# Performance work log

Measured on AMD Instinct MI355X. Metric: run time of the kernel, lower is better.

The kernel has to match this reference:

```python
import jax, jax.numpy as jnp
import numpy as np

B, S, H = 8, 2048, 512
M = 4096
TEMP = 0.1
EPS = 1e-6


def setup_inputs() -> dict:
    key = jax.random.key(0)
    ks = jax.random.split(key, 8)
    scale = 1.0 / np.sqrt(H)
    return {
        "hidden_states": jax.random.normal(ks[0], (B, S, H), dtype=jnp.float32),
        "memory_keys": jax.random.normal(ks[1], (M, H), dtype=jnp.float32),
        "memory_values": jax.random.normal(ks[2], (M, H), dtype=jnp.float32),
        "Wk": jax.random.normal(ks[3], (H, H), dtype=jnp.float32) * scale,
        "bk": jnp.zeros((H,), dtype=jnp.float32),
        "Wo": jax.random.normal(ks[4], (H, H), dtype=jnp.float32) * scale,
        "bo": jnp.zeros((H,), dtype=jnp.float32),
        "memory_usage": jax.random.randint(ks[5], (M,), 0, 2, dtype=jnp.int32),
    }


def reference(hidden_states, memory_keys, memory_values, Wk, bk, Wo, bo, memory_usage):
    # key projection: [B,S,H]
    q = jnp.einsum("bsh,kh->bsk", hidden_states, Wk) + bk
    # L2-style normalization with eps inside rsqrt (matches torch.rsqrt(norm_sq + 1e-6))
    q_n = q * jax.lax.rsqrt(jnp.sum(q * q, axis=-1, keepdims=True) + EPS)
    mk_n = memory_keys * jax.lax.rsqrt(
        jnp.sum(memory_keys * memory_keys, axis=-1, keepdims=True) + EPS
    )
    # cosine-similarity scores over the memory bank: [B,S,M]
    scores = jnp.einsum("bsk,mk->bsm", q_n, mk_n) / TEMP
    mask = (memory_usage > 0).astype(scores.dtype)  # [M]
    scores = scores * mask + (-1e9) * (1.0 - mask)
    attn = jax.nn.softmax(scores, axis=-1)  # [B,S,M]
    retrieved = jnp.einsum("bsm,mv->bsv", attn, memory_values)  # [B,S,H]
    out = jnp.einsum("bsv,hv->bsh", retrieved, Wo) + bo
    return out
```

## Files before the change

kernel.cpp:

```cpp
#include <hip/hip_runtime.h>
#include <cstdint>
#include <cstddef>

#define H_DIM   512
#define M_DIM   4096

typedef unsigned short u16;
typedef short bf16x8 __attribute__((ext_vector_type(8)));
typedef float f32x4  __attribute__((ext_vector_type(4)));

__device__ __forceinline__ u16 f2b(float f) {
  union { float f; uint32_t u; } v; v.f = f;
  uint32_t u = v.u + (0x7FFFu + ((v.u >> 16) & 1u));
  return (u16)(u >> 16);
}

__device__ __forceinline__ bf16x8 cvt8(const float4& lo, const float4& hi) {
  union { u16 u[8]; bf16x8 v; } o;
  o.u[0] = f2b(lo.x); o.u[1] = f2b(lo.y); o.u[2] = f2b(lo.z); o.u[3] = f2b(lo.w);
  o.u[4] = f2b(hi.x); o.u[5] = f2b(hi.y); o.u[6] = f2b(hi.z); o.u[7] = f2b(hi.w);
  return o.v;
}

__global__ void k_init(const float* __restrict__ wk, const float* __restrict__ wo,
                       u16* __restrict__ owk, u16* __restrict__ owo,
                       const int* __restrict__ usage, int* __restrict__ idx,
                       int* __restrict__ meta, float* __restrict__ lsum) {
  __shared__ int cnt[256];
  const int blk = blockIdx.x;
  const int t = threadIdx.x;
  if (blk < 512) {
    int i = blk * 256 + t;
    const float* src = (i < 65536) ? wk : wo;
    u16* dst = (i < 65536) ? owk : owo;
    int j = i & 65535;
    float4 v = ((const float4*)src)[j];
    ushort4 o;
    o.x = f2b(v.x); o.y = f2b(v.y); o.z = f2b(v.z); o.w = f2b(v.w);
    ((ushort4*)dst)[j] = o;
  } else if (blk == 512) {
    int base = t * 16;
    int c = 0;
    #pragma unroll
    for (int i = 0; i < 16; ++i) c += (usage[base + i] > 0) ? 1 : 0;
    cnt[t] = c;
    __syncthreads();
    for (int d = 1; d < 256; d <<= 1) {
      int v = (t >= d) ? cnt[t - d] : 0;
      __syncthreads();
      cnt[t] += v;
      __syncthreads();
    }
    int pos = cnt[t] - c;
    for (int i = 0; i < 16; ++i)
      if (usage[base + i] > 0) idx[pos++] = base + i;
    if (t == 0) {
      int total = cnt[255];
      int keff = ((total + 127) >> 7) << 7;
      meta[0] = total; meta[1] = keff; meta[2] = keff >> 5; meta[3] = keff >> 7;
    }
  } else {
    int i = (blk - 513) * 256 + t;
    float4 zf = {0.f, 0.f, 0.f, 0.f};
    ((float4*)lsum)[i] = zf;
  }
}

__global__ void k_gather_keys(const float* __restrict__ keys,
                              const int* __restrict__ idx, const int* __restrict__ meta,
                              u16* __restrict__ okeys) {
  int j    = blockIdx.x * 4 + (threadIdx.x >> 6);
  int lane = threadIdx.x & 63;
  int count = meta[0];
  ushort4* kp = (ushort4*)(okeys + (size_t)j * H_DIM);
  if (j >= count) {
    ushort4 z = {0, 0, 0, 0};
    kp[lane] = z; kp[lane + 64] = z;
    return;
  }
  int src = idx[j];
  const float4* rp = (const float4*)(keys + (size_t)src * H_DIM);
  float4 a = rp[lane];
  float4 b = rp[lane + 64];
  float ss = a.x*a.x + a.y*a.y + a.z*a.z + a.w*a.w
           + b.x*b.x + b.y*b.y + b.z*b.z + b.w*b.w;
  #pragma unroll
  for (int d = 1; d < 64; d <<= 1) ss += __shfl_xor(ss, d, 64);
  float s = rsqrtf(ss + 1e-6f);
  ushort4 oa, ob;
  oa.x = f2b(a.x*s); oa.y = f2b(a.y*s); oa.z = f2b(a.z*s); oa.w = f2b(a.w*s);
  ob.x = f2b(b.x*s); ob.y = f2b(b.y*s); ob.z = f2b(b.z*s); ob.w = f2b(b.w*s);
  kp[lane]      = oa;
  kp[lane + 64] = ob;
}

__global__ __launch_bounds__(256, 3)
void k_gemm_mw(const u16* __restrict__ A, const float* __restrict__ Bf,
               const int* __restrict__ idx, const int* __restrict__ meta,
               u16* __restrict__ outh) {
  __shared__ u16 Ah[2][128 * 32];
  __shared__ u16 Bh[2][128 * 32];

  const int tid  = threadIdx.x;
  const int wave = tid >> 6, lane = tid & 63;
  const int wr = (wave >> 1) * 64;
  const int wc = (wave & 1) * 64;

  const int count = meta[0];
  if (blockIdx.x >= (meta[1] >> 7)) return;
  const int row0 = blockIdx.y << 7;
  const int col0 = blockIdx.x << 7;
  const int kiters = 512 >> 5;

  const int srow   = lane & 15;
  const int schunk = lane >> 4;
  const int lds_off = schunk * 128 + srow * 8;

  const int fr = lane & 15;
  const int fbase = (lane >> 4) * 128 + fr * 8;
  const int g = lane >> 4;

  const char* Ac = (const char*)A;

  uint32_t aB[2];
  uint32_t bB[2];
  bool bval[2];
  #pragma unroll
  for (int s2 = 0; s2 < 2; ++s2) {
    aB[s2] = (uint32_t)(((size_t)(row0 + (wave + s2 * 4) * 16 + srow) * 512u
                         + (size_t)(schunk * 8)) * 2u);
    int mrow = col0 + (wave + s2 * 4) * 16 + srow;
    bval[s2] = (mrow < count);
    int src = bval[s2] ? idx[mrow] : 0;
    bB[s2] = (uint32_t)(((size_t)src * 512u + (size_t)(schunk * 8)) * 4u);
  }

  f32x4 acc[4][4];
  const f32x4 z = {0.0f, 0.0f, 0.0f, 0.0f};
  #pragma unroll
  for (int i = 0; i < 4; ++i)
    #pragma unroll
    for (int j = 0; j < 4; ++j) acc[i][j] = z;

  bf16x8 rA[2];
  float4 rBlo[2], rBhi[2];
  auto gload = [&](int k0) {
    const uint32_t kb  = (uint32_t)(k0 << 1);
    const uint32_t kbf = (uint32_t)(k0 << 2);
    #pragma unroll
    for (int s2 = 0; s2 < 2; ++s2) rA[s2] = *(const bf16x8*)(Ac + aB[s2] + kb);
    #pragma unroll
    for (int s2 = 0; s2 < 2; ++s2) {
      rBlo[s2] = *(const float4*)((const char*)Bf + bB[s2] + kbf);
      rBhi[s2] = *(const float4*)((const char*)Bf + bB[s2] + kbf + 16);
    }
  };

  const float4 zf = {0.f, 0.f, 0.f, 0.f};
  gload(0);
  for (int it = 0; it < kiters; ++it) {
    const int cur = it & 1;
    #pragma unroll
    for (int s2 = 0; s2 < 2; ++s2)
      *(bf16x8*)&Ah[cur][(wave + s2 * 4) * 512 + lds_off] = rA[s2];
    #pragma unroll
    for (int s2 = 0; s2 < 2; ++s2)
      *(bf16x8*)&Bh[cur][(wave + s2 * 4) * 512 + lds_off] =
          bval[s2] ? cvt8(rBlo[s2], rBhi[s2]) : cvt8(zf, zf);
    if (it + 1 < kiters) gload((it + 1) << 5);
    __syncthreads();

    bf16x8 af[4], bfv[4];
    #pragma unroll
    for (int i = 0; i < 4; ++i)
      af[i] = *(const bf16x8*)&Ah[cur][((wr >> 4) + i) * 512 + fbase];
    #pragma unroll
    for (int j = 0; j < 4; ++j)
      bfv[j] = *(const bf16x8*)&Bh[cur][((wc >> 4) + j) * 512 + fbase];
    #pragma unroll
    for (int i = 0; i < 4; ++i)
      #pragma unroll
      for (int j = 0; j < 4; ++j)
        acc[i][j] = __builtin_amdgcn_mfma_f32_16x16x32_bf16(af[i], bfv[j], acc[i][j], 0, 0, 0);
  }

  #pragma unroll
  for (int i = 0; i < 4; ++i) {
    #pragma unroll
    for (int r = 0; r < 4; ++r) {
      int grow = row0 + wr + i * 16 + g * 4 + r;
      #pragma unroll
      for (int j = 0; j < 4; ++j) {
        int gcol = col0 + wc + j * 16 + fr;
        outh[(size_t)grow * (size_t)M_DIM + gcol] = f2b(acc[i][j][r]);
      }
    }
  }
}

#define EPI2_P     0
#define EPI2_OUT   1
#define EPI2_QPROJ 2

template<int EPI>
__global__ __launch_bounds__(512, 2)
void k_gemm2(const u16* __restrict__ A, const u16* __restrict__ B,
             const int* __restrict__ meta,
             float* __restrict__ outf, u16* __restrict__ outh,
             const float* __restrict__ bias,
             float* __restrict__ aux,
             const float* __restrict__ rowscale) {
  constexpr int BM   = (EPI == EPI2_P) ? 256 : 128;
  constexpr int MF   = BM / 32;
  constexpr int NF   = 4;
  constexpr int APS  = BM / 128;
  constexpr int NLA  = BM / 64;
  constexpr int NLB  = 4;
  constexpr int ASUB = BM * 32;
  constexpr int BSUB = 256 * 32;
  constexpr bool BF32 = (EPI == EPI2_QPROJ);

  __shared__ u16 Ah[2][BM * 64];
  __shared__ u16 Bh[2][256 * 64];

  const int tid  = threadIdx.x;
  const int wave = tid >> 6, lane = tid & 63;
  const int wave_m = wave >> 2, wave_n = wave & 3;
  const int wm0 = wave_m * (BM >> 1);
  const int wn0 = wave_n * 64;
  const int fr  = lane & 15, g = lane >> 4;
  const int fbase = g * 128 + fr * 8;

  int m0, r0, kel;
  if (EPI == EPI2_P) {
    int id = blockIdx.x + (blockIdx.y << 4);
    int xcd = id & 7, s = id >> 3;
    r0 = (xcd * 8 + (s >> 4)) << 8;
    m0 = (s & 15) << 8;
    if (m0 >= meta[1]) return;
    kel = 512;
  } else if (EPI == EPI2_OUT) {
    int id = blockIdx.x + (blockIdx.y << 2);
    int xcd = id & 7, s = id >> 3;
    r0 = (xcd * 8 + (s >> 2)) << 8;
    m0 = (s & 3) << 7;
    kel = meta[1];
  } else {
    int id = blockIdx.x + (blockIdx.y << 2);
    int xcd = id & 7, s = id >> 3;
    r0 = (xcd * 8 + (s >> 2)) << 8;
    m0 = (s & 3) << 7;
    kel = 512;
  }
  const int kiters = kel >> 6;
  if (kiters <= 0) return;
  const int kstr = (EPI == EPI2_OUT) ? M_DIM : 512;

  const char* Ac = (const char*)A;
  const char* Bc = (const char*)B;
  uint32_t aB[NLA], bB[NLB];
  #pragma unroll
  for (int s2 = 0; s2 < NLA; ++s2) {
    int ks = s2 / APS;
    int u  = tid + (s2 % APS) * 512;
    int row = ((u >> 6) << 4) + (u & 15);
    int kch = (u >> 4) & 3;
    aB[s2] = (uint32_t)(((size_t)(m0 + row) * (size_t)kstr
                         + (size_t)(ks * 32 + kch * 8)) * 2u);
  }
  #pragma unroll
  for (int s2 = 0; s2 < NLB; ++s2) {
    int ks = s2 >> 1;
    int u  = tid + (s2 & 1) * 512;
    int row = ((u >> 6) << 4) + (u & 15);
    int kch = (u >> 4) & 3;
    bB[s2] = (uint32_t)(((size_t)(r0 + row) * (size_t)kstr
                         + (size_t)(ks * 32 + kch * 8)) * (BF32 ? 4u : 2u));
  }

  f32x4 acc[MF][NF];
  const f32x4 z = {0.0f, 0.0f, 0.0f, 0.0f};
  #pragma unroll
  for (int i = 0; i < MF; ++i)
    #pragma unroll
    for (int j = 0; j < NF; ++j) acc[i][j] = z;

  auto gloadA = [&](bf16x8 (&ra)[NLA], int it1) {
    const uint32_t kb = (uint32_t)(it1 << 7);
    #pragma unroll
    for (int s2 = 0; s2 < NLA; ++s2) ra[s2] = *(const bf16x8*)(Ac + aB[s2] + kb);
  };
  auto gloadBh = [&](bf16x8 (&rb)[NLB], int it1) {
    const uint32_t kb = (uint32_t)(it1 << 7);
    #pragma unroll
    for (int s2 = 0; s2 < NLB; ++s2) rb[s2] = *(const bf16x8*)(Bc + bB[s2] + kb);
  };
  auto gloadBf = [&](float4 (&lo)[NLB], float4 (&hi)[NLB], int it1) {
    const uint32_t kb = (uint32_t)(it1 << 8);
    #pragma unroll
    for (int s2 = 0; s2 < NLB; ++s2) {
      lo[s2] = *(const float4*)(Bc + bB[s2] + kb);
      hi[s2] = *(const float4*)(Bc + bB[s2] + kb + 16);
    }
  };
  auto commitA = [&](int cur, bf16x8 (&ra)[NLA]) {
    #pragma unroll
    for (int s2 = 0; s2 < NLA; ++s2)
      *(bf16x8*)&Ah[cur][(s2 / APS) * ASUB + (tid + (s2 % APS) * 512) * 8] = ra[s2];
  };
  auto commitBh = [&](int cur, bf16x8 (&rb)[NLB]) {
    #pragma unroll
    for (int s2 = 0; s2 < NLB; ++s2)
      *(bf16x8*)&Bh[cur][(s2 >> 1) * BSUB + (tid + (s2 & 1) * 512) * 8] = rb[s2];
  };
  auto commitBf = [&](int cur, float4 (&lo)[NLB], float4 (&hi)[NLB]) {
    #pragma unroll
    for (int s2 = 0; s2 < NLB; ++s2)
      *(bf16x8*)&Bh[cur][(s2 >> 1) * BSUB + (tid + (s2 & 1) * 512) * 8] =
          cvt8(lo[s2], hi[s2]);
  };
  auto compute = [&](int cur) {
    bf16x8 af[MF], bfv[NF];
    #pragma unroll
    for (int i = 0; i < MF; ++i)
      af[i] = *(const bf16x8*)&Ah[cur][((wm0 >> 4) + i) * 512 + fbase];
    #pragma unroll
    for (int j = 0; j < NF; ++j)
      bfv[j] = *(const bf16x8*)&Bh[cur][((wn0 >> 4) + j) * 512 + fbase];
    #pragma unroll
    for (int i = 0; i < MF; ++i)
      #pragma unroll
      for (int j = 0; j < NF; ++j)
        acc[i][j] = __builtin_amdgcn_mfma_f32_16x16x32_bf16(af[i], bfv[j], acc[i][j], 0, 0, 0);
    #pragma unroll
    for (int i = 0; i < MF; ++i)
      af[i] = *(const bf16x8*)&Ah[cur][ASUB + ((wm0 >> 4) + i) * 512 + fbase];
    #pragma unroll
    for (int j = 0; j < NF; ++j)
      bfv[j] = *(const bf16x8*)&Bh[cur][BSUB + ((wn0 >> 4) + j) * 512 + fbase];
    #pragma unroll
    for (int i = 0; i < MF; ++i)
      #pragma unroll
      for (int j = 0; j < NF; ++j)
        acc[i][j] = __builtin_amdgcn_mfma_f32_16x16x32_bf16(af[i], bfv[j], acc[i][j], 0, 0, 0);
  };

  if constexpr (EPI == EPI2_P) {
    bf16x8 rA[NLA], rB[NLB];
    gloadA(rA, 0); gloadBh(rB, 0);
    for (int it = 0; it < kiters; ++it) {
      const int cur = it & 1;
      commitA(cur, rA); commitBh(cur, rB);
      if (it + 1 < kiters) { gloadA(rA, it + 1); gloadBh(rB, it + 1); }
      __syncthreads();
      compute(cur);
    }
  } else if constexpr (!BF32) {
    bf16x8 a0[NLA], b0[NLB], a1[NLA], b1[NLB];
    gloadA(a0, 0); gloadBh(b0, 0);
    if (kiters > 1) { gloadA(a1, 1); gloadBh(b1, 1); }
    for (int it = 0; it < kiters; it += 2) {
      commitA(0, a0); commitBh(0, b0);
      if (it + 2 < kiters) { gloadA(a0, it + 2); gloadBh(b0, it + 2); }
      __syncthreads();
      compute(0);
      commitA(1, a1); commitBh(1, b1);
      if (it + 3 < kiters) { gloadA(a1, it + 3); gloadBh(b1, it + 3); }
      __syncthreads();
      compute(1);
    }
  } else {
    bf16x8 a0[NLA], a1[NLA];
    float4 b0lo[NLB], b0hi[NLB], b1lo[NLB], b1hi[NLB];
    gloadA(a0, 0); gloadBf(b0lo, b0hi, 0);
    if (kiters > 1) { gloadA(a1, 1); gloadBf(b1lo, b1hi, 1); }
    for (int it = 0; it < kiters; it += 2) {
      commitA(0, a0); commitBf(0, b0lo, b0hi);
      if (it + 2 < kiters) { gloadA(a0, it + 2); gloadBf(b0lo, b0hi, it + 2); }
      __syncthreads();
      compute(0);
      commitA(1, a1); commitBf(1, b1lo, b1hi);
      if (it + 3 < kiters) { gloadA(a1, it + 3); gloadBf(b1lo, b1hi, it + 3); }
      __syncthreads();
      compute(1);
    }
  }

  if (EPI == EPI2_P) {
    const int count = meta[0];
    float rq10[NF];
    #pragma unroll
    for (int j = 0; j < NF; ++j) {
      const size_t rr = (size_t)(r0 + wn0 + j * 16 + fr);
      float ssum = 0.0f;
      #pragma unroll
      for (int i = 0; i < 8; ++i) ssum += rowscale[rr * 8 + i];
      rq10[j] = rsqrtf(ssum + 1e-6f) * 10.0f;
    }
    float sj[NF] = {0.f, 0.f, 0.f, 0.f};
    #pragma unroll
    for (int i = 0; i < MF; ++i) {
      const int mb = m0 + wm0 + i * 16 + g * 4;
      #pragma unroll
      for (int j = 0; j < NF; ++j) {
        const size_t rr = (size_t)(r0 + wn0 + j * 16 + fr);
        float p0 = (mb + 0 < count) ? __expf(acc[i][j][0] * rq10[j]) : 0.0f;
        float p1 = (mb + 1 < count) ? __expf(acc[i][j][1] * rq10[j]) : 0.0f;
        float p2 = (mb + 2 < count) ? __expf(acc[i][j][2] * rq10[j]) : 0.0f;
        float p3 = (mb + 3 < count) ? __expf(acc[i][j][3] * rq10[j]) : 0.0f;
        ushort4 st; st.x = f2b(p0); st.y = f2b(p1); st.z = f2b(p2); st.w = f2b(p3);
        *(ushort4*)(outh + rr * M_DIM + mb) = st;
        sj[j] += (p0 + p1) + (p2 + p3);
      }
    }
    #pragma unroll
    for (int j = 0; j < NF; ++j) {
      float s = sj[j];
      s += __shfl_xor(s, 16, 64);
      s += __shfl_xor(s, 32, 64);
      if (lane < 16)
        atomicAdd(&aux[(size_t)(r0 + wn0 + j * 16 + lane)], s);
    }
  } else if (EPI == EPI2_OUT) {
    float scl[NF];
    #pragma unroll
    for (int j = 0; j < NF; ++j)
      scl[j] = 1.0f / rowscale[r0 + wn0 + j * 16 + fr];
    #pragma unroll
    for (int i = 0; i < MF; ++i) {
      const int hb = m0 + wm0 + i * 16 + g * 4;
      const float4 bv = *(const float4*)(bias + hb);
      #pragma unroll
      for (int j = 0; j < NF; ++j) {
        const size_t rr = (size_t)(r0 + wn0 + j * 16 + fr);
        float4 o;
        o.x = acc[i][j][0] * scl[j] + bv.x;
        o.y = acc[i][j][1] * scl[j] + bv.y;
        o.z = acc[i][j][2] * scl[j] + bv.z;
        o.w = acc[i][j][3] * scl[j] + bv.w;
        *(float4*)(outf + rr * H_DIM + hb) = o;
      }
    }
  } else {
    float sj[NF] = {0.f, 0.f, 0.f, 0.f};
    #pragma unroll
    for (int i = 0; i < MF; ++i) {
      const int kb = m0 + wm0 + i * 16 + g * 4;
      const float4 bkv = *(const float4*)(bias + kb);
      #pragma unroll
      for (int j = 0; j < NF; ++j) {
        const size_t rr = (size_t)(r0 + wn0 + j * 16 + fr);
        float v0 = acc[i][j][0] + bkv.x;
        float v1 = acc[i][j][1] + bkv.y;
        float v2 = acc[i][j][2] + bkv.z;
        float v3 = acc[i][j][3] + bkv.w;
        ushort4 st; st.x = f2b(v0); st.y = f2b(v1); st.z = f2b(v2); st.w = f2b(v3);
        *(ushort4*)(outh + rr * H_DIM + kb) = st;
        sj[j] += v0 * v0 + v1 * v1 + v2 * v2 + v3 * v3;
      }
    }
    const int slot = (m0 + wm0) >> 6;
    #pragma unroll
    for (int j = 0; j < NF; ++j) {
      float s = sj[j];
      s += __shfl_xor(s, 16, 64);
      s += __shfl_xor(s, 32, 64);
      if (lane < 16)
        aux[(size_t)(r0 + wn0 + j * 16 + lane) * 8 + slot] = s;
    }
  }
}

extern "C" void kernel_launch(void* const* d_in, const int* in_sizes, int n_in,
                              void* d_out, int out_size, void* d_ws, size_t ws_size,
                              hipStream_t stream) {
  const float* hidden = (const float*)d_in[0];
  const float* mkeys  = (const float*)d_in[1];
  const float* mvals  = (const float*)d_in[2];
  const float* Wk     = (const float*)d_in[3];
  const float* bk     = (const float*)d_in[4];
  const float* Wo     = (const float*)d_in[5];
  const float* bo     = (const float*)d_in[6];
  const int*   usage  = (const int*)d_in[7];
  (void)in_sizes; (void)n_in; (void)out_size; (void)ws_size;

  char* ws = (char*)d_ws;
  int*   idx   = (int*)(ws + 0);
  int*   meta  = (int*)(ws + 16384);
  float* lsum  = (float*)(ws + 1048576);
  float* qss   = (float*)(ws + 5242880);
  u16*   wkb   = (u16*)(ws + 16777216);
  u16*   wob   = (u16*)(ws + 17301504);
  u16*   mkn   = (u16*)(ws + 17825792);
  u16*   qb    = (u16*)(ws + 26214400);
  u16*   MWt   = (u16*)(ws + 42991616);
  u16*   P     = (u16*)(ws + 47185920);

  k_init<<<529, 256, 0, stream>>>(Wk, Wo, wkb, wob, usage, idx, meta, lsum);

  k_gather_keys<<<1024, 256, 0, stream>>>(mkeys, idx, meta, mkn);

  k_gemm2<EPI2_QPROJ><<<dim3(4, 64), 512, 0, stream>>>(wkb, (const u16*)hidden,
      nullptr, nullptr, qb, bk, qss, nullptr);

  k_gemm_mw<<<dim3(16, 4), 256, 0, stream>>>(wob, mvals, idx, meta, MWt);

  k_gemm2<EPI2_P><<<dim3(16, 64), 512, 0, stream>>>(mkn, qb, meta,
      nullptr, P, nullptr, lsum, qss);

  k_gemm2<EPI2_OUT><<<dim3(4, 64), 512, 0, stream>>>(MWt, P, meta,
      (float*)d_out, nullptr, bo, nullptr, lsum);
}
```

Measured before the change: 245.5 us.

## Merge key gather, Q projection, and MW gemm into one heterogeneous launch

Three independent middle-stage kernels (normalize/gather memory keys, Q projection GEMM, Wo·values GEMM) are combined into a single kernel that dispatches on block index. This removes two launch gaps and lets the small, under-occupying kernels run concurrently with the Q projection instead of serially. The cost is that every block now uses 512 threads and the largest shared-memory footprint, so half the threads idle in the MW blocks and occupancy for the gather blocks may drop.

```diff
diff --git a/kernel.cpp b/kernel.cpp
--- a/kernel.cpp
+++ b/kernel.cpp
@@ -66,141 +66,295 @@
   }
 }
 
-__global__ void k_gather_keys(const float* __restrict__ keys,
-                              const int* __restrict__ idx, const int* __restrict__ meta,
-                              u16* __restrict__ okeys) {
-  int j    = blockIdx.x * 4 + (threadIdx.x >> 6);
-  int lane = threadIdx.x & 63;
-  int count = meta[0];
-  ushort4* kp = (ushort4*)(okeys + (size_t)j * H_DIM);
-  if (j >= count) {
-    ushort4 z = {0, 0, 0, 0};
-    kp[lane] = z; kp[lane + 64] = z;
-    return;
-  }
-  int src = idx[j];
-  const float4* rp = (const float4*)(keys + (size_t)src * H_DIM);
-  float4 a = rp[lane];
-  float4 b = rp[lane + 64];
-  float ss = a.x*a.x + a.y*a.y + a.z*a.z + a.w*a.w
-           + b.x*b.x + b.y*b.y + b.z*b.z + b.w*b.w;
-  #pragma unroll
-  for (int d = 1; d < 64; d <<= 1) ss += __shfl_xor(ss, d, 64);
-  float s = rsqrtf(ss + 1e-6f);
-  ushort4 oa, ob;
-  oa.x = f2b(a.x*s); oa.y = f2b(a.y*s); oa.z = f2b(a.z*s); oa.w = f2b(a.w*s);
-  ob.x = f2b(b.x*s); ob.y = f2b(b.y*s); ob.z = f2b(b.z*s); ob.w = f2b(b.w*s);
-  kp[lane]      = oa;
-  kp[lane + 64] = ob;
-}
-
-__global__ __launch_bounds__(256, 3)
-void k_gemm_mw(const u16* __restrict__ A, const float* __restrict__ Bf,
-               const int* __restrict__ idx, const int* __restrict__ meta,
-               u16* __restrict__ outh) {
-  __shared__ u16 Ah[2][128 * 32];
-  __shared__ u16 Bh[2][128 * 32];
-
-  const int tid  = threadIdx.x;
-  const int wave = tid >> 6, lane = tid & 63;
-  const int wr = (wave >> 1) * 64;
-  const int wc = (wave & 1) * 64;
-
-  const int count = meta[0];
-  if (blockIdx.x >= (meta[1] >> 7)) return;
-  const int row0 = blockIdx.y << 7;
-  const int col0 = blockIdx.x << 7;
-  const int kiters = 512 >> 5;
-
-  const int srow   = lane & 15;
-  const int schunk = lane >> 4;
-  const int lds_off = schunk * 128 + srow * 8;
-
-  const int fr = lane & 15;
-  const int fbase = (lane >> 4) * 128 + fr * 8;
-  const int g = lane >> 4;
-
-  const char* Ac = (const char*)A;
-
-  uint32_t aB[2];
-  uint32_t bB[2];
-  bool bval[2];
-  #pragma unroll
-  for (int s2 = 0; s2 < 2; ++s2) {
-    aB[s2] = (uint32_t)(((size_t)(row0 + (wave + s2 * 4) * 16 + srow) * 512u
-                         + (size_t)(schunk * 8)) * 2u);
-    int mrow = col0 + (wave + s2 * 4) * 16 + srow;
-    bval[s2] = (mrow < count);
-    int src = bval[s2] ? idx[mrow] : 0;
-    bB[s2] = (uint32_t)(((size_t)src * 512u + (size_t)(schunk * 8)) * 4u);
-  }
-
-  f32x4 acc[4][4];
-  const f32x4 z = {0.0f, 0.0f, 0.0f, 0.0f};
-  #pragma unroll
-  for (int i = 0; i < 4; ++i)
-    #pragma unroll
-    for (int j = 0; j < 4; ++j) acc[i][j] = z;
-
-  bf16x8 rA[2];
-  float4 rBlo[2], rBhi[2];
-  auto gload = [&](int k0) {
-    const uint32_t kb  = (uint32_t)(k0 << 1);
-    const uint32_t kbf = (uint32_t)(k0 << 2);
-    #pragma unroll
-    for (int s2 = 0; s2 < 2; ++s2) rA[s2] = *(const bf16x8*)(Ac + aB[s2] + kb);
-    #pragma unroll
-    for (int s2 = 0; s2 < 2; ++s2) {
-      rBlo[s2] = *(const float4*)((const char*)Bf + bB[s2] + kbf);
-      rBhi[s2] = *(const float4*)((const char*)Bf + bB[s2] + kbf + 16);
-    }
-  };
-
-  const float4 zf = {0.f, 0.f, 0.f, 0.f};
-  gload(0);
-  for (int it = 0; it < kiters; ++it) {
-    const int cur = it & 1;
-    #pragma unroll
-    for (int s2 = 0; s2 < 2; ++s2)
-      *(bf16x8*)&Ah[cur][(wave + s2 * 4) * 512 + lds_off] = rA[s2];
-    #pragma unroll
-    for (int s2 = 0; s2 < 2; ++s2)
-      *(bf16x8*)&Bh[cur][(wave + s2 * 4) * 512 + lds_off] =
-          bval[s2] ? cvt8(rBlo[s2], rBhi[s2]) : cvt8(zf, zf);
-    if (it + 1 < kiters) gload((it + 1) << 5);
-    __syncthreads();
-
-    bf16x8 af[4], bfv[4];
+__global__ __launch_bounds__(512, 2)
+void k_mid(const u16* __restrict__ wkb, const float* __restrict__ hidden,
+           u16* __restrict__ qb, const float* __restrict__ bk,
+           float* __restrict__ qss,
+           const u16* __restrict__ wob, const float* __restrict__ mvals,
+           const int* __restrict__ idx, const int* __restrict__ meta,
+           u16* __restrict__ MWt,
+           const float* __restrict__ mkeys, u16* __restrict__ mkn) {
+  __shared__ u16 smem[49152];
+  const int blk = blockIdx.x;
+  const int tid = threadIdx.x;
+  const int lane = tid & 63;
+
+  if (blk < 256) {
+    constexpr int NLA  = 2;
+    constexpr int NLB  = 4;
+    constexpr int ASUB = 128 * 32;
+    constexpr int BSUB = 256 * 32;
+    u16* AhB = smem;
+    u16* BhB = smem + 16384;
+
+    const int wave = tid >> 6;
+    const int wave_m = wave >> 2, wave_n = wave & 3;
+    const int wm0 = wave_m * 64;
+    const int wn0 = wave_n * 64;
+    const int fr  = lane & 15, g = lane >> 4;
+    const int fbase = g * 128 + fr * 8;
+
+    int id = blk;
+    int xcd = id & 7, s = id >> 3;
+    const int r0 = (xcd * 8 + (s >> 2)) << 8;
+    const int m0 = (s & 3) << 7;
+    const int kiters = 512 >> 6;
+
+    const char* Ac = (const char*)wkb;
+    uint32_t aB[NLA], bB[NLB];
+    #pragma unroll
+    for (int s2 = 0; s2 < NLA; ++s2) {
+      int u  = tid;
+      int row = ((u >> 6) << 4) + (u & 15);
+      int kch = (u >> 4) & 3;
+      aB[s2] = (uint32_t)(((size_t)(m0 + row) * 512u
+                           + (size_t)(s2 * 32 + kch * 8)) * 2u);
+    }
+    #pragma unroll
+    for (int s2 = 0; s2 < NLB; ++s2) {
+      int ks = s2 >> 1;
+      int u  = tid + (s2 & 1) * 512;
+      int row = ((u >> 6) << 4) + (u & 15);
+      int kch = (u >> 4) & 3;
+      bB[s2] = (uint32_t)(((size_t)(r0 + row) * 512u
+                           + (size_t)(ks * 32 + kch * 8)) * 4u);
+    }
+
+    f32x4 acc[4][4];
+    const f32x4 z = {0.0f, 0.0f, 0.0f, 0.0f};
     #pragma unroll
     for (int i = 0; i < 4; ++i)
-      af[i] = *(const bf16x8*)&Ah[cur][((wr >> 4) + i) * 512 + fbase];
-    #pragma unroll
-    for (int j = 0; j < 4; ++j)
-      bfv[j] = *(const bf16x8*)&Bh[cur][((wc >> 4) + j) * 512 + fbase];
+      #pragma unroll
+      for (int j = 0; j < 4; ++j) acc[i][j] = z;
+
+    auto gloadA = [&](bf16x8 (&ra)[NLA], int it1) {
+      const uint32_t kb = (uint32_t)(it1 << 7);
+      #pragma unroll
+      for (int s2 = 0; s2 < NLA; ++s2) ra[s2] = *(const bf16x8*)(Ac + aB[s2] + kb);
+    };
+    auto gloadBf = [&](float4 (&lo)[NLB], float4 (&hi)[NLB], int it1) {
+      const uint32_t kb = (uint32_t)(it1 << 8);
+      #pragma unroll
+      for (int s2 = 0; s2 < NLB; ++s2) {
+        lo[s2] = *(const float4*)((const char*)hidden + bB[s2] + kb);
+        hi[s2] = *(const float4*)((const char*)hidden + bB[s2] + kb + 16);
+      }
+    };
+    auto commitA = [&](int cur, bf16x8 (&ra)[NLA]) {
+      #pragma unroll
+      for (int s2 = 0; s2 < NLA; ++s2)
+        *(bf16x8*)&AhB[cur * 8192 + s2 * ASUB + tid * 8] = ra[s2];
+    };
+    auto commitBf = [&](int cur, float4 (&lo)[NLB], float4 (&hi)[NLB]) {
+      #pragma unroll
+      for (int s2 = 0; s2 < NLB; ++s2)
+        *(bf16x8*)&BhB[cur * 16384 + (s2 >> 1) * BSUB + (tid + (s2 & 1) * 512) * 8] =
+            cvt8(lo[s2], hi[s2]);
+    };
+    auto compute = [&](int cur) {
+      bf16x8 af[4], bfv[4];
+      #pragma unroll
+      for (int i = 0; i < 4; ++i)
+        af[i] = *(const bf16x8*)&AhB[cur * 8192 + ((wm0 >> 4) + i) * 512 + fbase];
+      #pragma unroll
+      for (int j = 0; j < 4; ++j)
+        bfv[j] = *(const bf16x8*)&BhB[cur * 16384 + ((wn0 >> 4) + j) * 512 + fbase];
+      #pragma unroll
+      for (int i = 0; i < 4; ++i)
+        #pragma unroll
+        for (int j = 0; j < 4; ++j)
+          acc[i][j] = __builtin_amdgcn_mfma_f32_16x16x32_bf16(af[i], bfv[j], acc[i][j], 0, 0, 0);
+      #pragma unroll
+      for (int i = 0; i < 4; ++i)
+        af[i] = *(const bf16x8*)&AhB[cur * 8192 + ASUB + ((wm0 >> 4) + i) * 512 + fbase];
+      #pragma unroll
+      for (int j = 0; j < 4; ++j)
+        bfv[j] = *(const bf16x8*)&BhB[cur * 16384 + BSUB + ((wn0 >> 4) + j) * 512 + fbase];
+      #pragma unroll
+      for (int i = 0; i < 4; ++i)
+        #pragma unroll
+        for (int j = 0; j < 4; ++j)
+          acc[i][j] = __builtin_amdgcn_mfma_f32_16x16x32_bf16(af[i], bfv[j], acc[i][j], 0, 0, 0);
+    };
+
+    bf16x8 a0[NLA], a1[NLA];
+    float4 b0lo[NLB], b0hi[NLB], b1lo[NLB], b1hi[NLB];
+    gloadA(a0, 0); gloadBf(b0lo, b0hi, 0);
+    gloadA(a1, 1); gloadBf(b1lo, b1hi, 1);
+    for (int it = 0; it < kiters; it += 2) {
+      commitA(0, a0); commitBf(0, b0lo, b0hi);
+      if (it + 2 < kiters) { gloadA(a0, it + 2); gloadBf(b0lo, b0hi, it + 2); }
+      __syncthreads();
+      compute(0);
+      commitA(1, a1); commitBf(1, b1lo, b1hi);
+      if (it + 3 < kiters) { gloadA(a1, it + 3); gloadBf(b1lo, b1hi, it + 3); }
+      __syncthreads();
+      compute(1);
+    }
+
+    float sj[4] = {0.f, 0.f, 0.f, 0.f};
+    #pragma unroll
+    for (int i = 0; i < 4; ++i) {
+      const int kb = m0 + wm0 + i * 16 + g * 4;
+      const float4 bkv = *(const float4*)(bk + kb);
+      #pragma unroll
+      for (int j = 0; j < 4; ++j) {
+        const size_t rr = (size_t)(r0 + wn0 + j * 16 + fr);
+        float v0 = acc[i][j][0] + bkv.x;
+        float v1 = acc[i][j][1] + bkv.y;
+        float v2 = acc[i][j][2] + bkv.z;
+        float v3 = acc[i][j][3] + bkv.w;
+        ushort4 st; st.x = f2b(v0); st.y = f2b(v1); st.z = f2b(v2); st.w = f2b(v3);
+        *(ushort4*)(qb + rr * H_DIM + kb) = st;
+        sj[j] += v0 * v0 + v1 * v1 + v2 * v2 + v3 * v3;
+      }
+    }
+    const int slot = (m0 + wm0) >> 6;
+    #pragma unroll
+    for (int j = 0; j < 4; ++j) {
+      float s2 = sj[j];
+      s2 += __shfl_xor(s2, 16, 64);
+      s2 += __shfl_xor(s2, 32, 64);
+      if (lane < 16)
+        qss[(size_t)(r0 + wn0 + j * 16 + lane) * 8 + slot] = s2;
+    }
+
+  } else if (blk < 320) {
+    const int mb_blk = (blk - 256) & 15;
+    const int hb_blk = (blk - 256) >> 4;
+    if (mb_blk >= (meta[1] >> 7)) return;
+    const bool act = (tid < 256);
+
+    u16* AhB = smem;
+    u16* BhB = smem + 8192;
+
+    const int t256 = tid & 255;
+    const int wave = t256 >> 6;
+    const int wr = (wave >> 1) * 64;
+    const int wc = (wave & 1) * 64;
+    const int count = meta[0];
+    const int row0 = hb_blk << 7;
+    const int col0 = mb_blk << 7;
+    const int kiters = 512 >> 5;
+
+    const int srow   = lane & 15;
+    const int schunk = lane >> 4;
+    const int lds_off = schunk * 128 + srow * 8;
+    const int fr = lane & 15;
+    const int fbase = (lane >> 4) * 128 + fr * 8;
+    const int g = lane >> 4;
+
+    const char* Ac = (const char*)wob;
+
+    uint32_t aB[2], bB[2];
+    bool bval[2] = {false, false};
+    if (act) {
+      #pragma unroll
+      for (int s2 = 0; s2 < 2; ++s2) {
+        aB[s2] = (uint32_t)(((size_t)(row0 + (wave + s2 * 4) * 16 + srow) * 512u
+                             + (size_t)(schunk * 8)) * 2u);
+        int mrow = col0 + (wave + s2 * 4) * 16 + srow;
+        bval[s2] = (mrow < count);
+        int src = bval[s2] ? idx[mrow] : 0;
+        bB[s2] = (uint32_t)(((size_t)src * 512u + (size_t)(schunk * 8)) * 4u);
+      }
+    }
+
+    f32x4 acc[4][4];
+    const f32x4 z = {0.0f, 0.0f, 0.0f, 0.0f};
     #pragma unroll
     for (int i = 0; i < 4; ++i)
       #pragma unroll
-      for (int j = 0; j < 4; ++j)
-        acc[i][j] = __builtin_amdgcn_mfma_f32_16x16x32_bf16(af[i], bfv[j], acc[i][j], 0, 0, 0);
-  }
-
-  #pragma unroll
-  for (int i = 0; i < 4; ++i) {
-    #pragma unroll
-    for (int r = 0; r < 4; ++r) {
-      int grow = row0 + wr + i * 16 + g * 4 + r;
-      #pragma unroll
-      for (int j = 0; j < 4; ++j) {
-        int gcol = col0 + wc + j * 16 + fr;
-        outh[(size_t)grow * (size_t)M_DIM + gcol] = f2b(acc[i][j][r]);
-      }
-    }
+      for (int j = 0; j < 4; ++j) acc[i][j] = z;
+
+    bf16x8 rA[2];
+    float4 rBlo[2], rBhi[2];
+    auto gload = [&](int k0) {
+      const uint32_t kb  = (uint32_t)(k0 << 1);
+      const uint32_t kbf = (uint32_t)(k0 << 2);
+      #pragma unroll
+      for (int s2 = 0; s2 < 2; ++s2) rA[s2] = *(const bf16x8*)(Ac + aB[s2] + kb);
+      #pragma unroll
+      for (int s2 = 0; s2 < 2; ++s2) {
+        rBlo[s2] = *(const float4*)((const char*)mvals + bB[s2] + kbf);
+        rBhi[s2] = *(const float4*)((const char*)mvals + bB[s2] + kbf + 16);
+      }
+    };
+
+    const float4 zf = {0.f, 0.f, 0.f, 0.f};
+    if (act) gload(0);
+    for (int it = 0; it < kiters; ++it) {
+      const int cur = it & 1;
+      if (act) {
+        #pragma unroll
+        for (int s2 = 0; s2 < 2; ++s2)
+          *(bf16x8*)&AhB[cur * 4096 + (wave + s2 * 4) * 512 + lds_off] = rA[s2];
+        #pragma unroll
+        for (int s2 = 0; s2 < 2; ++s2)
+          *(bf16x8*)&BhB[cur * 4096 + (wave + s2 * 4) * 512 + lds_off] =
+              bval[s2] ? cvt8(rBlo[s2], rBhi[s2]) : cvt8(zf, zf);
+        if (it + 1 < kiters) gload((it + 1) << 5);
+      }
+      __syncthreads();
+      if (act) {
+        bf16x8 af[4], bfv[4];
+        #pragma unroll
+        for (int i = 0; i < 4; ++i)
+          af[i] = *(const bf16x8*)&AhB[cur * 4096 + ((wr >> 4) + i) * 512 + fbase];
+        #pragma unroll
+        for (int j = 0; j < 4; ++j)
+          bfv[j] = *(const bf16x8*)&BhB[cur * 4096 + ((wc >> 4) + j) * 512 + fbase];
+        #pragma unroll
+        for (int i = 0; i < 4; ++i)
+          #pragma unroll
+          for (int j = 0; j < 4; ++j)
+            acc[i][j] = __builtin_amdgcn_mfma_f32_16x16x32_bf16(af[i], bfv[j], acc[i][j], 0, 0, 0);
+      }
+    }
+
+    if (act) {
+      #pragma unroll
+      for (int i = 0; i < 4; ++i) {
+        #pragma unroll
+        for (int r = 0; r < 4; ++r) {
+          int grow = row0 + wr + i * 16 + g * 4 + r;
+          #pragma unroll
+          for (int j = 0; j < 4; ++j) {
+            int gcol = col0 + wc + j * 16 + fr;
+            MWt[(size_t)grow * (size_t)M_DIM + gcol] = f2b(acc[i][j][r]);
+          }
+        }
+      }
+    }
+
+  } else {
+    int j = (blk - 320) * 8 + (tid >> 6);
+    int count = meta[0];
+    ushort4* kp = (ushort4*)(mkn + (size_t)j * H_DIM);
+    if (j >= count) {
+      ushort4 zz = {0, 0, 0, 0};
+      kp[lane] = zz; kp[lane + 64] = zz;
+      return;
+    }
+    int src = idx[j];
+    const float4* rp = (const float4*)(mkeys + (size_t)src * H_DIM);
+    float4 a = rp[lane];
+    float4 b = rp[lane + 64];
+    float ss = a.x*a.x + a.y*a.y + a.z*a.z + a.w*a.w
+             + b.x*b.x + b.y*b.y + b.z*b.z + b.w*b.w;
+    #pragma unroll
+    for (int d = 1; d < 64; d <<= 1) ss += __shfl_xor(ss, d, 64);
+    float s = rsqrtf(ss + 1e-6f);
+    ushort4 oa, ob;
+    oa.x = f2b(a.x*s); oa.y = f2b(a.y*s); oa.z = f2b(a.z*s); oa.w = f2b(a.w*s);
+    ob.x = f2b(b.x*s); ob.y = f2b(b.y*s); ob.z = f2b(b.z*s); ob.w = f2b(b.w*s);
+    kp[lane]      = oa;
+    kp[lane + 64] = ob;
   }
 }
 
 #define EPI2_P     0
 #define EPI2_OUT   1
-#define EPI2_QPROJ 2
 
 template<int EPI>
 __global__ __launch_bounds__(512, 2)
@@ -218,7 +372,6 @@
   constexpr int NLB  = 4;
   constexpr int ASUB = BM * 32;
   constexpr int BSUB = 256 * 32;
-  constexpr bool BF32 = (EPI == EPI2_QPROJ);
 
   __shared__ u16 Ah[2][BM * 64];
   __shared__ u16 Bh[2][256 * 64];
@@ -239,18 +392,12 @@
     m0 = (s & 15) << 8;
     if (m0 >= meta[1]) return;
     kel = 512;
-  } else if (EPI == EPI2_OUT) {
+  } else {
     int id = blockIdx.x + (blockIdx.y << 2);
     int xcd = id & 7, s = id >> 3;
     r0 = (xcd * 8 + (s >> 2)) << 8;
     m0 = (s & 3) << 7;
     kel = meta[1];
-  } else {
-    int id = blockIdx.x + (blockIdx.y << 2);
-    int xcd = id & 7, s = id >> 3;
-    r0 = (xcd * 8 + (s >> 2)) << 8;
-    m0 = (s & 3) << 7;
-    kel = 512;
   }
   const int kiters = kel >> 6;
   if (kiters <= 0) return;
@@ -275,7 +422,7 @@
     int row = ((u >> 6) << 4) + (u & 15);
     int kch = (u >> 4) & 3;
     bB[s2] = (uint32_t)(((size_t)(r0 + row) * (size_t)kstr
-                         + (size_t)(ks * 32 + kch * 8)) * (BF32 ? 4u : 2u));
+                         + (size_t)(ks * 32 + kch * 8)) * 2u);
   }
 
   f32x4 acc[MF][NF];
@@ -295,14 +442,6 @@
     #pragma unroll
     for (int s2 = 0; s2 < NLB; ++s2) rb[s2] = *(const bf16x8*)(Bc + bB[s2] + kb);
   };
-  auto gloadBf = [&](float4 (&lo)[NLB], float4 (&hi)[NLB], int it1) {
-    const uint32_t kb = (uint32_t)(it1 << 8);
-    #pragma unroll
-    for (int s2 = 0; s2 < NLB; ++s2) {
-      lo[s2] = *(const float4*)(Bc + bB[s2] + kb);
-      hi[s2] = *(const float4*)(Bc + bB[s2] + kb + 16);
-    }
-  };
   auto commitA = [&](int cur, bf16x8 (&ra)[NLA]) {
     #pragma unroll
     for (int s2 = 0; s2 < NLA; ++s2)
@@ -312,12 +451,6 @@
     #pragma unroll
     for (int s2 = 0; s2 < NLB; ++s2)
       *(bf16x8*)&Bh[cur][(s2 >> 1) * BSUB + (tid + (s2 & 1) * 512) * 8] = rb[s2];
-  };
-  auto commitBf = [&](int cur, float4 (&lo)[NLB], float4 (&hi)[NLB]) {
-    #pragma unroll
-    for (int s2 = 0; s2 < NLB; ++s2)
-      *(bf16x8*)&Bh[cur][(s2 >> 1) * BSUB + (tid + (s2 & 1) * 512) * 8] =
-          cvt8(lo[s2], hi[s2]);
   };
   auto compute = [&](int cur) {
     bf16x8 af[MF], bfv[NF];
@@ -355,7 +488,7 @@
       __syncthreads();
       compute(cur);
     }
-  } else if constexpr (!BF32) {
+  } else {
     bf16x8 a0[NLA], b0[NLB], a1[NLA], b1[NLB];
     gloadA(a0, 0); gloadBh(b0, 0);
     if (kiters > 1) { gloadA(a1, 1); gloadBh(b1, 1); }
@@ -366,21 +499,6 @@
       compute(0);
       commitA(1, a1); commitBh(1, b1);
       if (it + 3 < kiters) { gloadA(a1, it + 3); gloadBh(b1, it + 3); }
-      __syncthreads();
-      compute(1);
-    }
-  } else {
-    bf16x8 a0[NLA], a1[NLA];
-    float4 b0lo[NLB], b0hi[NLB], b1lo[NLB], b1hi[NLB];
-    gloadA(a0, 0); gloadBf(b0lo, b0hi, 0);
-    if (kiters > 1) { gloadA(a1, 1); gloadBf(b1lo, b1hi, 1); }
-    for (int it = 0; it < kiters; it += 2) {
-      commitA(0, a0); commitBf(0, b0lo, b0hi);
-      if (it + 2 < kiters) { gloadA(a0, it + 2); gloadBf(b0lo, b0hi, it + 2); }
-      __syncthreads();
-      compute(0);
-      commitA(1, a1); commitBf(1, b1lo, b1hi);
-      if (it + 3 < kiters) { gloadA(a1, it + 3); gloadBf(b1lo, b1hi, it + 3); }
       __syncthreads();
       compute(1);
     }
@@ -421,7 +539,7 @@
       if (lane < 16)
         atomicAdd(&aux[(size_t)(r0 + wn0 + j * 16 + lane)], s);
     }
-  } else if (EPI == EPI2_OUT) {
+  } else {
     float scl[NF];
     #pragma unroll
     for (int j = 0; j < NF; ++j)
@@ -440,33 +558,6 @@
         o.w = acc[i][j][3] * scl[j] + bv.w;
         *(float4*)(outf + rr * H_DIM + hb) = o;
       }
-    }
-  } else {
-    float sj[NF] = {0.f, 0.f, 0.f, 0.f};
-    #pragma unroll
-    for (int i = 0; i < MF; ++i) {
-      const int kb = m0 + wm0 + i * 16 + g * 4;
-      const float4 bkv = *(const float4*)(bias + kb);
-      #pragma unroll
-      for (int j = 0; j < NF; ++j) {
-        const size_t rr = (size_t)(r0 + wn0 + j * 16 + fr);
-        float v0 = acc[i][j][0] + bkv.x;
-        float v1 = acc[i][j][1] + bkv.y;
-        float v2 = acc[i][j][2] + bkv.z;
-        float v3 = acc[i][j][3] + bkv.w;
-        ushort4 st; st.x = f2b(v0); st.y = f2b(v1); st.z = f2b(v2); st.w = f2b(v3);
-        *(ushort4*)(outh + rr * H_DIM + kb) = st;
-        sj[j] += v0 * v0 + v1 * v1 + v2 * v2 + v3 * v3;
-      }
-    }
-    const int slot = (m0 + wm0) >> 6;
-    #pragma unroll
-    for (int j = 0; j < NF; ++j) {
-      float s = sj[j];
-      s += __shfl_xor(s, 16, 64);
-      s += __shfl_xor(s, 32, 64);
-      if (lane < 16)
-        aux[(size_t)(r0 + wn0 + j * 16 + lane) * 8 + slot] = s;
     }
   }
 }
@@ -498,12 +589,9 @@
 
   k_init<<<529, 256, 0, stream>>>(Wk, Wo, wkb, wob, usage, idx, meta, lsum);
 
-  k_gather_keys<<<1024, 256, 0, stream>>>(mkeys, idx, meta, mkn);
-
-  k_gemm2<EPI2_QPROJ><<<dim3(4, 64), 512, 0, stream>>>(wkb, (const u16*)hidden,
-      nullptr, nullptr, qb, bk, qss, nullptr);
-
-  k_gemm_mw<<<dim3(16, 4), 256, 0, stream>>>(wob, mvals, idx, meta, MWt);
+  k_mid<<<832, 512, 0, stream>>>(wkb, hidden, qb, bk, qss,
+                                 wob, mvals, idx, meta, MWt,
+                                 mkeys, mkn);
 
   k_gemm2<EPI2_P><<<dim3(16, 64), 512, 0, stream>>>(mkn, qb, meta,
       nullptr, P, nullptr, lsum, qss);
```

Result: no change. 243.6 us (-0.8%).
